# Optimization experiments

Hardware: AMD Instinct MI355X
Metric: run time of the kernel (lower is better)

Reference implementation:

```python
import jax, jax.numpy as jnp
import numpy as np

B, N, S, K = 4, 32768, 8192, 16
IN_C, OUT_C = 64, 128
MID = max(OUT_C // 4, 8)  # attn_mlp hidden = 32
GN_GROUPS = 8
EPS = 1e-5


def setup_inputs() -> dict:
    key = jax.random.key(0)
    ks = jax.random.split(key, 16)
    def lin(k, out_c, in_c):
        # torch nn.Linear default init: U(-1/sqrt(in), 1/sqrt(in)), weight shape (out, in)
        bound = 1.0 / np.sqrt(in_c)
        return jax.random.uniform(k, (out_c, in_c), jnp.float32, -bound, bound)
    return {
        "xyz": jax.random.normal(ks[0], (B, N, 3), jnp.float32),
        "feats": jax.random.normal(ks[1], (B, N, IN_C), jnp.float32),
        "idx_fps": jax.random.randint(ks[2], (B, S), 0, N),
        "idx_knn": jax.random.randint(ks[3], (B, S, K), 0, N),
        "Wq": lin(ks[4], OUT_C, IN_C),
        "Wk": lin(ks[5], OUT_C, IN_C),
        "Wv": lin(ks[6], OUT_C, IN_C),
        "Wp1": lin(ks[7], OUT_C, 3),
        "Wp2": lin(ks[8], OUT_C, OUT_C),
        "Wa1": lin(ks[9], MID, OUT_C),
        "Wa2": lin(ks[10], OUT_C, MID),
        "Wproj": lin(ks[11], OUT_C, OUT_C),
        "ln_w": jnp.ones((OUT_C,), jnp.float32),
        "ln_b": jnp.zeros((OUT_C,), jnp.float32),
        "Wres": lin(ks[12], OUT_C, IN_C),
        "Wpost": lin(ks[13], OUT_C, OUT_C),
        "gn_w": jnp.ones((OUT_C,), jnp.float32),
        "gn_b": jnp.zeros((OUT_C,), jnp.float32),
    }


def _gather(x, idx):
    # x: (B, N, C); idx: (B, ...) -> (B, ..., C)
    return jax.vmap(lambda xb, ib: xb[ib])(x, idx)


def _layer_norm(x, w, b):
    mu = x.mean(-1, keepdims=True)
    var = x.var(-1, keepdims=True)
    return (x - mu) * jax.lax.rsqrt(var + EPS) * w + b


def _group_norm(x, w, b):
    # x: (B, S, C); normalize per (batch, group) over (S, C//G) — matches GroupNorm on (B,C,L)
    Bx, Sx, C = x.shape
    xg = x.reshape(Bx, Sx, GN_GROUPS, C // GN_GROUPS)
    mu = xg.mean(axis=(1, 3), keepdims=True)
    var = xg.var(axis=(1, 3), keepdims=True)
    xn = (xg - mu) * jax.lax.rsqrt(var + EPS)
    return xn.reshape(Bx, Sx, C) * w + b


def _forward(xyz, feats, idx_fps, idx_knn, Wq, Wk, Wv, Wp1, Wp2, Wa1, Wa2,
             Wproj, ln_w, ln_b, Wres, Wpost, gn_w, gn_b):
    s_xyz = _gather(xyz, idx_fps)        # (B,S,3)
    s_feat = _gather(feats, idx_fps)     # (B,S,C_in)
    n_xyz = _gather(xyz, idx_knn)        # (B,S,k,3)
    n_feat = _gather(feats, idx_knn)     # (B,S,k,C_in)

    # LocalAttentionBlock (Point Transformer v1 subtraction attention)
    q = jnp.einsum('bsc,oc->bso', s_feat, Wq)[:, :, None, :]   # (B,S,1,O)
    kk = jnp.einsum('bskc,oc->bsko', n_feat, Wk)               # (B,S,k,O)
    v = jnp.einsum('bskc,oc->bsko', n_feat, Wv)
    rel = n_xyz - s_xyz[:, :, None, :]                         # (B,S,k,3)
    pe = jnp.einsum('bskm,om->bsko',
                    jax.nn.relu(jnp.einsum('bskc,oc->bsko', rel, Wp1)), Wp2)
    h = q - kk + pe
    w = jnp.einsum('bskm,om->bsko',
                   jax.nn.relu(jnp.einsum('bsko,mo->bskm', h, Wa1)), Wa2)
    w = jax.nn.softmax(w, axis=2)                              # softmax over k
    out = jnp.sum(w * (v + pe), axis=2)                        # (B,S,O)
    out = jnp.einsum('bso,po->bsp', out, Wproj)
    res = jnp.einsum('bsc,oc->bso', s_feat, Wres)
    out = _layer_norm(out + res, ln_w, ln_b)

    # post: Conv1d(1x1, no bias) -> GroupNorm(8) -> ReLU
    out = jnp.einsum('bso,po->bsp', out, Wpost)
    out = jax.nn.relu(_group_norm(out, gn_w, gn_b))
    return s_xyz, out


def reference(xyz, feats, idx_fps, idx_knn, Wq, Wk, Wv, Wp1, Wp2, Wa1, Wa2,
              Wproj, ln_w, ln_b, Wres, Wpost, gn_w, gn_b):
    return _forward(xyz, feats, idx_fps, idx_knn, Wq, Wk, Wv, Wp1, Wp2, Wa1,
                    Wa2, Wproj, ln_w, ln_b, Wres, Wpost, gn_w, gn_b)
```

## Files before the change

kernel.cpp:

```cpp
#include <hip/hip_runtime.h>
#include <hip/hip_bf16.h>
#include <math.h>

#define B_ 4
#define N_ 32768
#define S_ 8192
#define K_ 16
#define CIN 64
#define COUT 128
#define MID_ 32
#define EPS_ 1e-5f
#define NTILE 2048

typedef __attribute__((ext_vector_type(8))) short s16x8;
typedef __attribute__((ext_vector_type(4))) float f32x4;

__device__ ushort g_attn[(size_t)B_ * S_ * COUT];
__device__ ushort g_sfeat[(size_t)B_ * S_ * CIN];
__device__ float  g_part[NTILE * 8 * 2];
__device__ float  g_stats[64];
__device__ float  g_fw[8192];

__device__ __forceinline__ uint pk2(float lo, float hi) {
  __hip_bfloat162 h = __float22bfloat162_rn(make_float2(lo, hi));
  return *(uint*)&h;
}
__device__ __forceinline__ ushort f2bf(float f) {
  __hip_bfloat16 h = __float2bfloat16(f);
  return *(ushort*)&h;
}
__device__ __forceinline__ int4 pack8(float4 a, float4 b) {
  int4 o;
  o.x = pk2(a.x, a.y); o.y = pk2(a.z, a.w);
  o.z = pk2(b.x, b.y); o.w = pk2(b.z, b.w);
  return o;
}
__device__ __forceinline__ f32x4 mfma16(s16x8 a, s16x8 b, f32x4 c) {
  return __builtin_amdgcn_mfma_f32_16x16x32_bf16(a, b, c, 0, 0, 0);
}
__device__ __forceinline__ s16x8 ldw256(const ushort* W, int row, int g) {
  return *(const s16x8*)((const char*)W + row * 256 + ((g ^ (row & 7)) << 4));
}
__device__ __forceinline__ s16x8 ldw128(const ushort* W, int row, int g) {
  return *(const s16x8*)((const char*)W + row * 128 + ((g ^ (row & 7)) << 4));
}
__device__ __forceinline__ s16x8 ldfrag_g8(const float* p) {
  float4 a = *(const float4*)p, b = *(const float4*)(p + 4);
  union { int4 i; s16x8 s; } u;
  u.i = pack8(a, b);
  return u.s;
}
__device__ __forceinline__ void st16(char* bufb, int t, f32x4 c, int l, int cq,
                                     bool dorelu) {
  const int colp = (l & 15) + 16 * t;
  const int g = colp >> 3;
  const int off = (colp & 7) * 2;
  #pragma unroll
  for (int rr = 0; rr < 4; ++rr) {
    const int row = cq * 4 + rr;
    float v = dorelu ? fmaxf(c[rr], 0.f) : c[rr];
    *(ushort*)(bufb + row * 256 + ((g ^ (row & 7)) << 4) + off) = f2bf(v);
  }
}
__device__ __forceinline__ void st16_a1(char* bufb, int t, f32x4 c, int l, int cq) {
  const int colp = (l & 15) + 16 * t;
  const int g = colp >> 3;
  const int off = (colp & 7) * 2;
  #pragma unroll
  for (int rr = 0; rr < 4; ++rr) {
    const int row = cq * 4 + rr;
    *(ushort*)(bufb + row * 64 + ((g ^ (row & 3)) << 4) + off) =
        f2bf(fmaxf(c[rr], 0.f));
  }
}

__global__ __launch_bounds__(256) void k_fuse(
    const float* __restrict__ Wq, const float* __restrict__ Wk,
    const float* __restrict__ Wp2, const float* __restrict__ Wa1)
{
  const int t = blockIdx.x * 256 + threadIdx.x;
  if (t < 2048) {
    int m = t >> 6, c = t & 63;
    float s = 0.f;
    for (int o = 0; o < COUT; ++o) s += Wa1[m * COUT + o] * Wq[o * CIN + c];
    g_fw[t] = s;
  } else if (t < 4096) {
    int u = t - 2048;
    int m = u >> 6, c = u & 63;
    float s = 0.f;
    for (int o = 0; o < COUT; ++o) s += Wa1[m * COUT + o] * Wk[o * CIN + c];
    g_fw[t] = s;
  } else {
    int u = t - 4096;
    int m = u >> 7, c = u & 127;
    float s = 0.f;
    for (int o = 0; o < COUT; ++o) s += Wa1[m * COUT + o] * Wp2[o * COUT + c];
    g_fw[t] = s;
  }
}

__global__ __launch_bounds__(512, 2) void k_attn(
    const float* __restrict__ xyz, const float* __restrict__ feats,
    const int* __restrict__ idx_fps, const int* __restrict__ idx_knn,
    const float* __restrict__ Wv, const float* __restrict__ Wp1,
    const float* __restrict__ Wp2, const float* __restrict__ Wa2,
    float* __restrict__ out_xyz)
{
  __shared__ ushort lWv[COUT * CIN];
  __shared__ ushort lWp1[COUT * 8];
  __shared__ ushort lWp2[COUT * COUT];
  __shared__ ushort lWka1[MID_ * CIN];
  __shared__ ushort lWpa1[MID_ * COUT];
  __shared__ ushort sbuf[8 * 2560];

  const int tid = threadIdx.x;
  const int w = tid >> 6, l = tid & 63;
  const int r = l & 15, cq = l >> 4;

  for (int i = tid; i < COUT * CIN / 2; i += 512) {
    int row = i >> 5; int kp = (i & 31) * 2;
    int g = kp >> 3;
    *(uint*)((char*)lWv + row * 128 + ((g ^ (row & 7)) << 4) + (kp & 7) * 2)
        = pk2(Wv[row * CIN + kp], Wv[row * CIN + kp + 1]);
  }
  {
    int row = tid >> 2; int kp = (tid & 3) * 2;
    float lo = (kp < 3) ? Wp1[row * 3 + kp] : 0.f;
    float hi = (kp + 1 < 3) ? Wp1[row * 3 + kp + 1] : 0.f;
    *(uint*)((char*)lWp1 + row * 16 + kp * 2) = pk2(lo, hi);
  }
  for (int i = tid; i < COUT * CIN; i += 512) {
    int row = i >> 6; int kp = (i & 63) * 2;
    int g = kp >> 3;
    *(uint*)((char*)lWp2 + row * 256 + ((g ^ (row & 7)) << 4) + (kp & 7) * 2)
        = pk2(Wp2[row * COUT + kp], Wp2[row * COUT + kp + 1]);
  }
  for (int i = tid; i < MID_ * CIN / 2; i += 512) {
    int row = i >> 5; int kp = (i & 31) * 2;
    int g = kp >> 3;
    const float* src = g_fw + 2048 + row * CIN + kp;
    *(uint*)((char*)lWka1 + row * 128 + ((g ^ (row & 7)) << 4) + (kp & 7) * 2)
        = pk2(-src[0], -src[1]);
  }
  for (int i = tid; i < MID_ * COUT / 2; i += 512) {
    int row = i >> 6; int kp = (i & 63) * 2;
    int g = kp >> 3;
    const float* src = g_fw + 4096 + row * COUT + kp;
    *(uint*)((char*)lWpa1 + row * 256 + ((g ^ (row & 7)) << 4) + (kp & 7) * 2)
        = pk2(src[0], src[1]);
  }

  s16x8 fWa2[8], fQ[2][2];
  #pragma unroll
  for (int t = 0; t < 8; ++t)
    fWa2[t] = ldfrag_g8(Wa2 + (16 * t + r) * MID_ + cq * 8);
  #pragma unroll
  for (int t = 0; t < 2; ++t)
    #pragma unroll
    for (int ks = 0; ks < 2; ++ks)
      fQ[t][ks] = ldfrag_g8(g_fw + (16 * t + r) * CIN + ks * 32 + cq * 8);

  __syncthreads();

  char* bufb = (char*)(sbuf + w * 2560);
  const int pid0 = (blockIdx.x * 8 + w) * 16;

  {
    const int p = pid0 + r;
    const int bb = p >> 13;
    const int si = idx_fps[p];
    const float* fs = feats + ((size_t)bb * N_ + si) * CIN;
    #pragma unroll
    for (int j = 0; j < 2; ++j) {
      int g = cq * 2 + j;
      int4 pks = pack8(*(const float4*)(fs + g * 8), *(const float4*)(fs + g * 8 + 4));
      *(int4*)(bufb + r * 128 + ((g ^ (r & 7)) << 4)) = pks;
      *(int4*)((char*)g_sfeat + (size_t)p * 128 + g * 16) = pks;
    }
    if (l < 48) {
      int pi = l / 3, j = l - pi * 3;
      int pp = pid0 + pi;
      out_xyz[(size_t)pp * 3 + j] =
          xyz[((size_t)(pp >> 13) * N_ + idx_fps[pp]) * 3 + j];
    }
  }
  f32x4 qa1[2];
  qa1[0] = (f32x4){0, 0, 0, 0}; qa1[1] = (f32x4){0, 0, 0, 0};
  {
    s16x8 fS[2];
    #pragma unroll
    for (int ks = 0; ks < 2; ++ks)
      fS[ks] = *(const s16x8*)(bufb + r * 128 + (((ks * 4 + cq) ^ (r & 7)) << 4));
    #pragma unroll
    for (int ks = 0; ks < 2; ++ks)
      #pragma unroll
      for (int t = 0; t < 2; ++t)
        qa1[t] = mfma16(fS[ks], fQ[t][ks], qa1[t]);
  }

  float4 pf0, pf1, pf2, pf3;
  float pxn0, pxn1, pxn2, pxs0, pxs1, pxs2;
  int nid_n;
  {
    int nid0 = idx_knn[(size_t)pid0 * K_ + r];
    const float* fn = feats + ((size_t)N_ * (pid0 >> 13) + nid0) * CIN + cq * 16;
    pf0 = ((const float4*)fn)[0]; pf1 = ((const float4*)fn)[1];
    pf2 = ((const float4*)fn)[2]; pf3 = ((const float4*)fn)[3];
    if (cq == 0) {
      const float* xn = xyz + ((size_t)N_ * (pid0 >> 13) + nid0) * 3;
      const float* xs = xyz + ((size_t)N_ * (pid0 >> 13) + idx_fps[pid0]) * 3;
      pxn0 = xn[0]; pxn1 = xn[1]; pxn2 = xn[2];
      pxs0 = xs[0]; pxs1 = xs[1]; pxs2 = xs[2];
    }
    nid_n = idx_knn[(size_t)(pid0 + 1) * K_ + r];
  }

  #pragma unroll 1
  for (int i = 0; i < 16; ++i) {
    const int pid = pid0 + i;

    {
      int g0 = cq * 2;
      *(int4*)(bufb + r * 128 + ((g0 ^ (r & 7)) << 4)) = pack8(pf0, pf1);
      *(int4*)(bufb + r * 128 + (((g0 + 1) ^ (r & 7)) << 4)) = pack8(pf2, pf3);
    }
    s16x8 fRel = {0, 0, 0, 0, 0, 0, 0, 0};
    if (cq == 0) {
      fRel[0] = (short)f2bf(pxn0 - pxs0);
      fRel[1] = (short)f2bf(pxn1 - pxs1);
      fRel[2] = (short)f2bf(pxn2 - pxs2);
    }

    if (i < 15) {
      const int pidn = pid + 1;
      const int bn = pidn >> 13;
      const float* fn = feats + ((size_t)bn * N_ + nid_n) * CIN + cq * 16;
      float4 t0 = ((const float4*)fn)[0], t1 = ((const float4*)fn)[1];
      float4 t2 = ((const float4*)fn)[2], t3 = ((const float4*)fn)[3];
      if (cq == 0) {
        const float* xn = xyz + ((size_t)bn * N_ + nid_n) * 3;
        const float* xs = xyz + ((size_t)bn * N_ + idx_fps[pidn]) * 3;
        pxn0 = xn[0]; pxn1 = xn[1]; pxn2 = xn[2];
        pxs0 = xs[0]; pxs1 = xs[1]; pxs2 = xs[2];
      }
      if (i < 14) nid_n = idx_knn[(size_t)(pid + 2) * K_ + r];
      pf0 = t0; pf1 = t1; pf2 = t2; pf3 = t3;
    }

    s16x8 fA[2];
    #pragma unroll
    for (int ks = 0; ks < 2; ++ks)
      fA[ks] = *(const s16x8*)(bufb + r * 128 + (((ks * 4 + cq) ^ (r & 7)) << 4));

    f32x4 vv[8];
    #pragma unroll
    for (int t = 0; t < 8; ++t) vv[t] = (f32x4){0, 0, 0, 0};
    #pragma unroll
    for (int ks = 0; ks < 2; ++ks)
      #pragma unroll
      for (int t = 0; t < 8; ++t)
        vv[t] = mfma16(fA[ks], ldw128(lWv, 16 * t + r, ks * 4 + cq), vv[t]);

    f32x4 za[2];
    za[0] = (f32x4){0, 0, 0, 0}; za[1] = (f32x4){0, 0, 0, 0};
    #pragma unroll
    for (int ks = 0; ks < 2; ++ks)
      #pragma unroll
      for (int t = 0; t < 2; ++t)
        za[t] = mfma16(fA[ks], ldw128(lWka1, 16 * t + r, ks * 4 + cq), za[t]);

    #pragma unroll
    for (int t = 0; t < 8; ++t) {
      f32x4 z = {0, 0, 0, 0};
      f32x4 c = mfma16(fRel, *(const s16x8*)((const char*)lWp1 + (16 * t + r) * 16), z);
      st16(bufb, t, c, l, cq, true);
    }
    s16x8 fT[4];
    #pragma unroll
    for (int ks = 0; ks < 4; ++ks)
      fT[ks] = *(const s16x8*)(bufb + r * 256 + (((ks * 4 + cq) ^ (r & 7)) << 4));

    #pragma unroll
    for (int ks = 0; ks < 4; ++ks)
      #pragma unroll
      for (int t = 0; t < 8; ++t)
        vv[t] = mfma16(fT[ks], ldw256(lWp2, 16 * t + r, ks * 4 + cq), vv[t]);

    #pragma unroll
    for (int ks = 0; ks < 4; ++ks)
      #pragma unroll
      for (int t = 0; t < 2; ++t)
        za[t] = mfma16(fT[ks], ldw256(lWpa1, 16 * t + r, ks * 4 + cq), za[t]);

    const int ii = i & 3, iq = i >> 2;
    #pragma unroll
    for (int t = 0; t < 2; ++t) {
      float qsel = ii == 0 ? qa1[t][0] : ii == 1 ? qa1[t][1]
                 : ii == 2 ? qa1[t][2] : qa1[t][3];
      float qv = __shfl(qsel, (iq << 4) + (l & 15));
      #pragma unroll
      for (int rr = 0; rr < 4; ++rr) za[t][rr] += qv;
      st16_a1(bufb + 4096, t, za[t], l, cq);
    }
    s16x8 fA1 = *(const s16x8*)(bufb + 4096 + r * 64 + ((cq ^ (r & 3)) << 4));
    f32x4 ww[8];
    #pragma unroll
    for (int t = 0; t < 8; ++t) {
      f32x4 z = {0, 0, 0, 0};
      ww[t] = mfma16(fA1, fWa2[t], z);
    }
    #pragma unroll
    for (int t = 0; t < 8; ++t) {
      float m = fmaxf(fmaxf(ww[t][0], ww[t][1]), fmaxf(ww[t][2], ww[t][3]));
      m = fmaxf(m, __shfl_xor(m, 16));
      m = fmaxf(m, __shfl_xor(m, 32));
      float e0 = __expf(ww[t][0] - m), e1 = __expf(ww[t][1] - m);
      float e2 = __expf(ww[t][2] - m), e3 = __expf(ww[t][3] - m);
      float ss = e0 + e1 + e2 + e3;
      ss += __shfl_xor(ss, 16);
      ss += __shfl_xor(ss, 32);
      float acc = e0 * vv[t][0] + e1 * vv[t][1] + e2 * vv[t][2] + e3 * vv[t][3];
      acc += __shfl_xor(acc, 16);
      acc += __shfl_xor(acc, 32);
      float outv = acc / ss;
      if (cq == (t >> 2)) {
        int colp = (l & 15) + 16 * t;
        *(ushort*)((char*)g_attn + (size_t)pid * 256 + colp * 2) = f2bf(outv);
      }
    }
  }
}

__global__ __launch_bounds__(512, 2) void k_post(
    const float* __restrict__ Wproj, const float* __restrict__ Wres,
    const float* __restrict__ Wpost, const float* __restrict__ ln_w,
    const float* __restrict__ ln_b, float* __restrict__ out_main)
{
  __shared__ ushort lWpj[COUT * COUT];
  __shared__ ushort lWrs[COUT * CIN];
  __shared__ ushort lWps[COUT * COUT];
  __shared__ float  llnw[COUT], llnb[COUT];
  __shared__ ushort sbuf[8 * 16 * COUT];

  const int tid = threadIdx.x;
  const int w = tid >> 6, l = tid & 63;
  const int r = l & 15, cq = l >> 4;

  for (int i = tid; i < COUT * CIN; i += 512) {
    int row = i >> 6; int kp = (i & 63) * 2;
    int g = kp >> 3;
    *(uint*)((char*)lWpj + row * 256 + ((g ^ (row & 7)) << 4) + (kp & 7) * 2)
        = pk2(Wproj[row * COUT + kp], Wproj[row * COUT + kp + 1]);
  }
  for (int i = tid; i < COUT * CIN / 2; i += 512) {
    int row = i >> 5; int kp = (i & 31) * 2;
    int g = kp >> 3;
    *(uint*)((char*)lWrs + row * 128 + ((g ^ (row & 7)) << 4) + (kp & 7) * 2)
        = pk2(Wres[row * CIN + kp], Wres[row * CIN + kp + 1]);
  }
  for (int i = tid; i < COUT * CIN; i += 512) {
    int row = i >> 6; int kp = (i & 63) * 2;
    int g = kp >> 3;
    *(uint*)((char*)lWps + row * 256 + ((g ^ (row & 7)) << 4) + (kp & 7) * 2)
        = pk2(Wpost[row * COUT + kp], Wpost[row * COUT + kp + 1]);
  }
  if (tid < COUT) { llnw[tid] = ln_w[tid]; llnb[tid] = ln_b[tid]; }
  __syncthreads();

  const int T = blockIdx.x * 8 + w;
  char* bufb = (char*)(sbuf + w * 16 * COUT);

  f32x4 acc[8];
  #pragma unroll
  for (int t = 0; t < 8; ++t) acc[t] = (f32x4){0, 0, 0, 0};

  s16x8 fA[4];
  #pragma unroll
  for (int ks = 0; ks < 4; ++ks)
    fA[ks] = *(const s16x8*)(g_attn + ((size_t)T * 16 + r) * COUT + ks * 32 + cq * 8);
  #pragma unroll
  for (int ks = 0; ks < 4; ++ks)
    #pragma unroll
    for (int t = 0; t < 8; ++t)
      acc[t] = mfma16(fA[ks], ldw256(lWpj, 16 * t + r, ks * 4 + cq), acc[t]);

  s16x8 fS[2];
  #pragma unroll
  for (int ks = 0; ks < 2; ++ks)
    fS[ks] = *(const s16x8*)(g_sfeat + ((size_t)T * 16 + r) * CIN + ks * 32 + cq * 8);
  #pragma unroll
  for (int ks = 0; ks < 2; ++ks)
    #pragma unroll
    for (int t = 0; t < 8; ++t)
      acc[t] = mfma16(fS[ks], ldw128(lWrs, 16 * t + r, ks * 4 + cq), acc[t]);

  #pragma unroll
  for (int rr = 0; rr < 4; ++rr) {
    float s1 = 0.f, s2 = 0.f;
    #pragma unroll
    for (int t = 0; t < 8; ++t) { float v = acc[t][rr]; s1 += v; s2 += v * v; }
    #pragma unroll
    for (int off = 1; off < 16; off <<= 1) {
      s1 += __shfl_xor(s1, off);
      s2 += __shfl_xor(s2, off);
    }
    float mu = s1 * (1.f / COUT);
    float rs = rsqrtf(s2 * (1.f / COUT) - mu * mu + EPS_);
    #pragma unroll
    for (int t = 0; t < 8; ++t) {
      int col = (l & 15) + 16 * t;
      acc[t][rr] = (acc[t][rr] - mu) * rs * llnw[col] + llnb[col];
    }
  }
  #pragma unroll
  for (int t = 0; t < 8; ++t) st16(bufb, t, acc[t], l, cq, false);

  s16x8 fZ[4];
  #pragma unroll
  for (int ks = 0; ks < 4; ++ks)
    fZ[ks] = *(const s16x8*)(bufb + r * 256 + (((ks * 4 + cq) ^ (r & 7)) << 4));
  f32x4 po[8];
  #pragma unroll
  for (int t = 0; t < 8; ++t) po[t] = (f32x4){0, 0, 0, 0};
  #pragma unroll
  for (int ks = 0; ks < 4; ++ks)
    #pragma unroll
    for (int t = 0; t < 8; ++t)
      po[t] = mfma16(fZ[ks], ldw256(lWps, 16 * t + r, ks * 4 + cq), po[t]);

  #pragma unroll
  for (int t = 0; t < 8; ++t) {
    float s1 = po[t][0] + po[t][1] + po[t][2] + po[t][3];
    float s2 = po[t][0] * po[t][0] + po[t][1] * po[t][1]
             + po[t][2] * po[t][2] + po[t][3] * po[t][3];
    #pragma unroll
    for (int off = 1; off < 64; off <<= 1) {
      s1 += __shfl_xor(s1, off);
      s2 += __shfl_xor(s2, off);
    }
    if (l == 0) {
      g_part[((size_t)T * 8 + t) * 2] = s1;
      g_part[((size_t)T * 8 + t) * 2 + 1] = s2;
    }
    #pragma unroll
    for (int rr = 0; rr < 4; ++rr) {
      int row = T * 16 + cq * 4 + rr;
      out_main[(size_t)row * COUT + (l & 15) + 16 * t] = po[t][rr];
    }
  }
}

__global__ void k_gn_finish(void) {
  int bg = blockIdx.x;
  int b = bg >> 3, g = bg & 7;
  int t = threadIdx.x;
  float s1 = 0.f, s2 = 0.f;
  for (int i = t; i < 512; i += 64) {
    size_t T = (size_t)b * 512 + i;
    s1 += g_part[(T * 8 + g) * 2];
    s2 += g_part[(T * 8 + g) * 2 + 1];
  }
  #pragma unroll
  for (int off = 1; off < 64; off <<= 1) {
    s1 += __shfl_xor(s1, off);
    s2 += __shfl_xor(s2, off);
  }
  if (t == 0) {
    float n = (float)S_ * 16.f;
    float mu = s1 / n;
    float var = s2 / n - mu * mu;
    g_stats[bg * 2] = mu;
    g_stats[bg * 2 + 1] = rsqrtf(var + EPS_);
  }
}

__global__ __launch_bounds__(256) void k_gn_apply(
    float* __restrict__ x, const float* __restrict__ gn_w,
    const float* __restrict__ gn_b)
{
  const int i = blockIdx.x * 256 + threadIdx.x;
  if (i >= B_ * S_ * (COUT / 4)) return;
  const int c = (i & 31) * 4;
  const int g = c >> 4;
  const int b = i >> 18;
  const float m = g_stats[(b * 8 + g) * 2];
  const float rv = g_stats[(b * 8 + g) * 2 + 1];
  float4 v = ((float4*)x)[i];
  v.x = fmaxf((v.x - m) * rv * gn_w[c + 0] + gn_b[c + 0], 0.f);
  v.y = fmaxf((v.y - m) * rv * gn_w[c + 1] + gn_b[c + 1], 0.f);
  v.z = fmaxf((v.z - m) * rv * gn_w[c + 2] + gn_b[c + 2], 0.f);
  v.w = fmaxf((v.w - m) * rv * gn_w[c + 3] + gn_b[c + 3], 0.f);
  ((float4*)x)[i] = v;
}

extern "C" void kernel_launch(void* const* d_in, const int* in_sizes, int n_in,
                              void* d_out, int out_size, void* d_ws, size_t ws_size,
                              hipStream_t stream) {
  const float* xyz     = (const float*)d_in[0];
  const float* feats   = (const float*)d_in[1];
  const int*   idx_fps = (const int*)d_in[2];
  const int*   idx_knn = (const int*)d_in[3];
  const float* Wq    = (const float*)d_in[4];
  const float* Wk    = (const float*)d_in[5];
  const float* Wv    = (const float*)d_in[6];
  const float* Wp1   = (const float*)d_in[7];
  const float* Wp2   = (const float*)d_in[8];
  const float* Wa1   = (const float*)d_in[9];
  const float* Wa2   = (const float*)d_in[10];
  const float* Wproj = (const float*)d_in[11];
  const float* ln_w  = (const float*)d_in[12];
  const float* ln_b  = (const float*)d_in[13];
  const float* Wres  = (const float*)d_in[14];
  const float* Wpost = (const float*)d_in[15];
  const float* gn_w  = (const float*)d_in[16];
  const float* gn_b  = (const float*)d_in[17];

  float* out      = (float*)d_out;
  float* out_xyz  = out;
  float* out_main = out + (size_t)B_ * S_ * 3;

  k_fuse<<<dim3(32), dim3(256), 0, stream>>>(Wq, Wk, Wp2, Wa1);
  k_attn<<<dim3(256), dim3(512), 0, stream>>>(
      xyz, feats, idx_fps, idx_knn, Wv, Wp1, Wp2, Wa2, out_xyz);
  k_post<<<dim3(256), dim3(512), 0, stream>>>(
      Wproj, Wres, Wpost, ln_w, ln_b, out_main);
  k_gn_finish<<<dim3(32), dim3(64), 0, stream>>>();
  k_gn_apply<<<dim3((B_ * S_ * (COUT / 4) + 255) / 256), dim3(256), 0, stream>>>(
      out_main, gn_w, gn_b);
}
```

Measured before the change: 140.5 us.

## Process two sample points per loop iteration in attention kernel

The attention kernel now handles two sample points per iteration, giving each wave two LDS buffers so each weight fragment loaded from LDS feeds two MFMAs. Prefetching becomes two-deep and the per-wave LDS buffer doubles. Launch bounds drop from two blocks per CU to one to make room for the extra registers and LDS. This trades occupancy for better weight reuse and more independent MFMA chains.

```diff
diff --git a/kernel.cpp b/kernel.cpp
--- a/kernel.cpp
+++ b/kernel.cpp
@@ -72,6 +72,23 @@
     *(ushort*)(bufb + row * 64 + ((g ^ (row & 3)) << 4) + off) =
         f2bf(fmaxf(c[rr], 0.f));
   }
+}
+
+struct PF { float4 f0, f1, f2, f3; float r0, r1, r2; };
+__device__ __forceinline__ PF pfetch(const float* feats, const float* xyz,
+                                     const int* idx_fps, int pid, int nid, int cq) {
+  PF p;
+  const int bb = pid >> 13;
+  const float* fn = feats + ((size_t)bb * N_ + nid) * CIN + cq * 16;
+  p.f0 = ((const float4*)fn)[0]; p.f1 = ((const float4*)fn)[1];
+  p.f2 = ((const float4*)fn)[2]; p.f3 = ((const float4*)fn)[3];
+  p.r0 = 0.f; p.r1 = 0.f; p.r2 = 0.f;
+  if (cq == 0) {
+    const float* xn = xyz + ((size_t)bb * N_ + nid) * 3;
+    const float* xs = xyz + ((size_t)bb * N_ + idx_fps[pid]) * 3;
+    p.r0 = xn[0] - xs[0]; p.r1 = xn[1] - xs[1]; p.r2 = xn[2] - xs[2];
+  }
+  return p;
 }
 
 __global__ __launch_bounds__(256) void k_fuse(
@@ -99,7 +116,7 @@
   }
 }
 
-__global__ __launch_bounds__(512, 2) void k_attn(
+__global__ __launch_bounds__(512, 1) void k_attn(
     const float* __restrict__ xyz, const float* __restrict__ feats,
     const int* __restrict__ idx_fps, const int* __restrict__ idx_knn,
     const float* __restrict__ Wv, const float* __restrict__ Wp1,
@@ -111,7 +128,7 @@
   __shared__ ushort lWp2[COUT * COUT];
   __shared__ ushort lWka1[MID_ * CIN];
   __shared__ ushort lWpa1[MID_ * COUT];
-  __shared__ ushort sbuf[8 * 2560];
+  __shared__ ushort sbuf[8 * 5120];
 
   const int tid = threadIdx.x;
   const int w = tid >> 6, l = tid & 63;
@@ -150,19 +167,18 @@
         = pk2(src[0], src[1]);
   }
 
-  s16x8 fWa2[8], fQ[2][2];
+  s16x8 fWa2[8];
   #pragma unroll
   for (int t = 0; t < 8; ++t)
     fWa2[t] = ldfrag_g8(Wa2 + (16 * t + r) * MID_ + cq * 8);
-  #pragma unroll
-  for (int t = 0; t < 2; ++t)
-    #pragma unroll
-    for (int ks = 0; ks < 2; ++ks)
-      fQ[t][ks] = ldfrag_g8(g_fw + (16 * t + r) * CIN + ks * 32 + cq * 8);
 
   __syncthreads();
 
-  char* bufb = (char*)(sbuf + w * 2560);
+  char* bufb = (char*)(sbuf + w * 5120);
+  char* buf0 = bufb;
+  char* buf1 = bufb + 4096;
+  char* bufa0 = bufb + 8192;
+  char* bufa1 = bufb + 9216;
   const int pid0 = (blockIdx.x * 8 + w) * 16;
 
   {
@@ -174,7 +190,7 @@
     for (int j = 0; j < 2; ++j) {
       int g = cq * 2 + j;
       int4 pks = pack8(*(const float4*)(fs + g * 8), *(const float4*)(fs + g * 8 + 4));
-      *(int4*)(bufb + r * 128 + ((g ^ (r & 7)) << 4)) = pks;
+      *(int4*)(buf0 + r * 128 + ((g ^ (r & 7)) << 4)) = pks;
       *(int4*)((char*)g_sfeat + (size_t)p * 128 + g * 16) = pks;
     }
     if (l < 48) {
@@ -187,145 +203,173 @@
   f32x4 qa1[2];
   qa1[0] = (f32x4){0, 0, 0, 0}; qa1[1] = (f32x4){0, 0, 0, 0};
   {
-    s16x8 fS[2];
+    s16x8 fS[2], fQ;
     #pragma unroll
     for (int ks = 0; ks < 2; ++ks)
-      fS[ks] = *(const s16x8*)(bufb + r * 128 + (((ks * 4 + cq) ^ (r & 7)) << 4));
+      fS[ks] = *(const s16x8*)(buf0 + r * 128 + (((ks * 4 + cq) ^ (r & 7)) << 4));
     #pragma unroll
     for (int ks = 0; ks < 2; ++ks)
       #pragma unroll
-      for (int t = 0; t < 2; ++t)
-        qa1[t] = mfma16(fS[ks], fQ[t][ks], qa1[t]);
-  }
-
-  float4 pf0, pf1, pf2, pf3;
-  float pxn0, pxn1, pxn2, pxs0, pxs1, pxs2;
-  int nid_n;
-  {
-    int nid0 = idx_knn[(size_t)pid0 * K_ + r];
-    const float* fn = feats + ((size_t)N_ * (pid0 >> 13) + nid0) * CIN + cq * 16;
-    pf0 = ((const float4*)fn)[0]; pf1 = ((const float4*)fn)[1];
-    pf2 = ((const float4*)fn)[2]; pf3 = ((const float4*)fn)[3];
-    if (cq == 0) {
-      const float* xn = xyz + ((size_t)N_ * (pid0 >> 13) + nid0) * 3;
-      const float* xs = xyz + ((size_t)N_ * (pid0 >> 13) + idx_fps[pid0]) * 3;
-      pxn0 = xn[0]; pxn1 = xn[1]; pxn2 = xn[2];
-      pxs0 = xs[0]; pxs1 = xs[1]; pxs2 = xs[2];
-    }
-    nid_n = idx_knn[(size_t)(pid0 + 1) * K_ + r];
-  }
+      for (int t = 0; t < 2; ++t) {
+        fQ = ldfrag_g8(g_fw + (16 * t + r) * CIN + ks * 32 + cq * 8);
+        qa1[t] = mfma16(fS[ks], fQ, qa1[t]);
+      }
+  }
+
+  PF pa = pfetch(feats, xyz, idx_fps, pid0,
+                 idx_knn[(size_t)pid0 * K_ + r], cq);
+  PF pb = pfetch(feats, xyz, idx_fps, pid0 + 1,
+                 idx_knn[(size_t)(pid0 + 1) * K_ + r], cq);
+  int nidA = idx_knn[(size_t)(pid0 + 2) * K_ + r];
+  int nidB = idx_knn[(size_t)(pid0 + 3) * K_ + r];
 
   #pragma unroll 1
-  for (int i = 0; i < 16; ++i) {
-    const int pid = pid0 + i;
+  for (int ip = 0; ip < 8; ++ip) {
+    const int pidA = pid0 + 2 * ip;
+    const int pidB = pidA + 1;
 
     {
       int g0 = cq * 2;
-      *(int4*)(bufb + r * 128 + ((g0 ^ (r & 7)) << 4)) = pack8(pf0, pf1);
-      *(int4*)(bufb + r * 128 + (((g0 + 1) ^ (r & 7)) << 4)) = pack8(pf2, pf3);
-    }
-    s16x8 fRel = {0, 0, 0, 0, 0, 0, 0, 0};
+      *(int4*)(buf0 + r * 128 + ((g0 ^ (r & 7)) << 4)) = pack8(pa.f0, pa.f1);
+      *(int4*)(buf0 + r * 128 + (((g0 + 1) ^ (r & 7)) << 4)) = pack8(pa.f2, pa.f3);
+      *(int4*)(buf1 + r * 128 + ((g0 ^ (r & 7)) << 4)) = pack8(pb.f0, pb.f1);
+      *(int4*)(buf1 + r * 128 + (((g0 + 1) ^ (r & 7)) << 4)) = pack8(pb.f2, pb.f3);
+    }
+    s16x8 fRa = {0, 0, 0, 0, 0, 0, 0, 0};
+    s16x8 fRb = {0, 0, 0, 0, 0, 0, 0, 0};
     if (cq == 0) {
-      fRel[0] = (short)f2bf(pxn0 - pxs0);
-      fRel[1] = (short)f2bf(pxn1 - pxs1);
-      fRel[2] = (short)f2bf(pxn2 - pxs2);
-    }
-
-    if (i < 15) {
-      const int pidn = pid + 1;
-      const int bn = pidn >> 13;
-      const float* fn = feats + ((size_t)bn * N_ + nid_n) * CIN + cq * 16;
-      float4 t0 = ((const float4*)fn)[0], t1 = ((const float4*)fn)[1];
-      float4 t2 = ((const float4*)fn)[2], t3 = ((const float4*)fn)[3];
-      if (cq == 0) {
-        const float* xn = xyz + ((size_t)bn * N_ + nid_n) * 3;
-        const float* xs = xyz + ((size_t)bn * N_ + idx_fps[pidn]) * 3;
-        pxn0 = xn[0]; pxn1 = xn[1]; pxn2 = xn[2];
-        pxs0 = xs[0]; pxs1 = xs[1]; pxs2 = xs[2];
-      }
-      if (i < 14) nid_n = idx_knn[(size_t)(pid + 2) * K_ + r];
-      pf0 = t0; pf1 = t1; pf2 = t2; pf3 = t3;
-    }
-
-    s16x8 fA[2];
-    #pragma unroll
-    for (int ks = 0; ks < 2; ++ks)
-      fA[ks] = *(const s16x8*)(bufb + r * 128 + (((ks * 4 + cq) ^ (r & 7)) << 4));
-
-    f32x4 vv[8];
-    #pragma unroll
-    for (int t = 0; t < 8; ++t) vv[t] = (f32x4){0, 0, 0, 0};
+      fRa[0] = (short)f2bf(pa.r0); fRa[1] = (short)f2bf(pa.r1);
+      fRa[2] = (short)f2bf(pa.r2);
+      fRb[0] = (short)f2bf(pb.r0); fRb[1] = (short)f2bf(pb.r1);
+      fRb[2] = (short)f2bf(pb.r2);
+    }
+
+    if (ip < 7) {
+      pa = pfetch(feats, xyz, idx_fps, pidA + 2, nidA, cq);
+      pb = pfetch(feats, xyz, idx_fps, pidB + 2, nidB, cq);
+      if (ip < 6) {
+        nidA = idx_knn[(size_t)(pidA + 4) * K_ + r];
+        nidB = idx_knn[(size_t)(pidB + 4) * K_ + r];
+      }
+    }
+
+    s16x8 fAa[2], fAb[2];
+    #pragma unroll
+    for (int ks = 0; ks < 2; ++ks) {
+      fAa[ks] = *(const s16x8*)(buf0 + r * 128 + (((ks * 4 + cq) ^ (r & 7)) << 4));
+      fAb[ks] = *(const s16x8*)(buf1 + r * 128 + (((ks * 4 + cq) ^ (r & 7)) << 4));
+    }
+
+    f32x4 va[8], vb[8];
+    #pragma unroll
+    for (int t = 0; t < 8; ++t) { va[t] = (f32x4){0,0,0,0}; vb[t] = (f32x4){0,0,0,0}; }
     #pragma unroll
     for (int ks = 0; ks < 2; ++ks)
       #pragma unroll
-      for (int t = 0; t < 8; ++t)
-        vv[t] = mfma16(fA[ks], ldw128(lWv, 16 * t + r, ks * 4 + cq), vv[t]);
-
-    f32x4 za[2];
-    za[0] = (f32x4){0, 0, 0, 0}; za[1] = (f32x4){0, 0, 0, 0};
+      for (int t = 0; t < 8; ++t) {
+        s16x8 wb = ldw128(lWv, 16 * t + r, ks * 4 + cq);
+        va[t] = mfma16(fAa[ks], wb, va[t]);
+        vb[t] = mfma16(fAb[ks], wb, vb[t]);
+      }
+
+    f32x4 zaa[2], zab[2];
+    zaa[0] = (f32x4){0,0,0,0}; zaa[1] = (f32x4){0,0,0,0};
+    zab[0] = (f32x4){0,0,0,0}; zab[1] = (f32x4){0,0,0,0};
     #pragma unroll
     for (int ks = 0; ks < 2; ++ks)
       #pragma unroll
-      for (int t = 0; t < 2; ++t)
-        za[t] = mfma16(fA[ks], ldw128(lWka1, 16 * t + r, ks * 4 + cq), za[t]);
+      for (int t = 0; t < 2; ++t) {
+        s16x8 wb = ldw128(lWka1, 16 * t + r, ks * 4 + cq);
+        zaa[t] = mfma16(fAa[ks], wb, zaa[t]);
+        zab[t] = mfma16(fAb[ks], wb, zab[t]);
+      }
 
     #pragma unroll
     for (int t = 0; t < 8; ++t) {
-      f32x4 z = {0, 0, 0, 0};
-      f32x4 c = mfma16(fRel, *(const s16x8*)((const char*)lWp1 + (16 * t + r) * 16), z);
-      st16(bufb, t, c, l, cq, true);
-    }
-    s16x8 fT[4];
-    #pragma unroll
-    for (int ks = 0; ks < 4; ++ks)
-      fT[ks] = *(const s16x8*)(bufb + r * 256 + (((ks * 4 + cq) ^ (r & 7)) << 4));
+      s16x8 wp = *(const s16x8*)((const char*)lWp1 + (16 * t + r) * 16);
+      f32x4 z0 = {0, 0, 0, 0}, z1 = {0, 0, 0, 0};
+      f32x4 ca = mfma16(fRa, wp, z0);
+      f32x4 cb = mfma16(fRb, wp, z1);
+      st16(buf0, t, ca, l, cq, true);
+      st16(buf1, t, cb, l, cq, true);
+    }
+    s16x8 fTa[4], fTb[4];
+    #pragma unroll
+    for (int ks = 0; ks < 4; ++ks) {
+      fTa[ks] = *(const s16x8*)(buf0 + r * 256 + (((ks * 4 + cq) ^ (r & 7)) << 4));
+      fTb[ks] = *(const s16x8*)(buf1 + r * 256 + (((ks * 4 + cq) ^ (r & 7)) << 4));
+    }
 
     #pragma unroll
     for (int ks = 0; ks < 4; ++ks)
       #pragma unroll
-      for (int t = 0; t < 8; ++t)
-        vv[t] = mfma16(fT[ks], ldw256(lWp2, 16 * t + r, ks * 4 + cq), vv[t]);
+      for (int t = 0; t < 8; ++t) {
+        s16x8 wb = ldw256(lWp2, 16 * t + r, ks * 4 + cq);
+        va[t] = mfma16(fTa[ks], wb, va[t]);
+        vb[t] = mfma16(fTb[ks], wb, vb[t]);
+      }
 
     #pragma unroll
     for (int ks = 0; ks < 4; ++ks)
       #pragma unroll
-      for (int t = 0; t < 2; ++t)
-        za[t] = mfma16(fT[ks], ldw256(lWpa1, 16 * t + r, ks * 4 + cq), za[t]);
-
-    const int ii = i & 3, iq = i >> 2;
-    #pragma unroll
-    for (int t = 0; t < 2; ++t) {
-      float qsel = ii == 0 ? qa1[t][0] : ii == 1 ? qa1[t][1]
-                 : ii == 2 ? qa1[t][2] : qa1[t][3];
-      float qv = __shfl(qsel, (iq << 4) + (l & 15));
+      for (int t = 0; t < 2; ++t) {
+        s16x8 wb = ldw256(lWpa1, 16 * t + r, ks * 4 + cq);
+        zaa[t] = mfma16(fTa[ks], wb, zaa[t]);
+        zab[t] = mfma16(fTb[ks], wb, zab[t]);
+      }
+
+    {
+      const int ja = 2 * ip, jb = 2 * ip + 1;
+      const int iia = ja & 3, iqa = ja >> 2;
+      const int iib = jb & 3, iqb = jb >> 2;
       #pragma unroll
-      for (int rr = 0; rr < 4; ++rr) za[t][rr] += qv;
-      st16_a1(bufb + 4096, t, za[t], l, cq);
-    }
-    s16x8 fA1 = *(const s16x8*)(bufb + 4096 + r * 64 + ((cq ^ (r & 3)) << 4));
-    f32x4 ww[8];
+      for (int t = 0; t < 2; ++t) {
+        float qsa = iia == 0 ? qa1[t][0] : iia == 1 ? qa1[t][1]
+                  : iia == 2 ? qa1[t][2] : qa1[t][3];
+        float qva = __shfl(qsa, (iqa << 4) + (l & 15));
+        float qsb = iib == 0 ? qa1[t][0] : iib == 1 ? qa1[t][1]
+                  : iib == 2 ? qa1[t][2] : qa1[t][3];
+        float qvb = __shfl(qsb, (iqb << 4) + (l & 15));
+        f32x4 ta = zaa[t], tb = zab[t];
+        #pragma unroll
+        for (int rr = 0; rr < 4; ++rr) { ta[rr] += qva; tb[rr] += qvb; }
+        st16_a1(bufa0, t, ta, l, cq);
+        st16_a1(bufa1, t, tb, l, cq);
+      }
+    }
+    s16x8 fA1a = *(const s16x8*)(bufa0 + r * 64 + ((cq ^ (r & 3)) << 4));
+    s16x8 fA1b = *(const s16x8*)(bufa1 + r * 64 + ((cq ^ (r & 3)) << 4));
+    f32x4 wwa[8], wwb[8];
     #pragma unroll
     for (int t = 0; t < 8; ++t) {
-      f32x4 z = {0, 0, 0, 0};
-      ww[t] = mfma16(fA1, fWa2[t], z);
+      f32x4 z0 = {0, 0, 0, 0}, z1 = {0, 0, 0, 0};
+      wwa[t] = mfma16(fA1a, fWa2[t], z0);
+      wwb[t] = mfma16(fA1b, fWa2[t], z1);
     }
     #pragma unroll
     for (int t = 0; t < 8; ++t) {
-      float m = fmaxf(fmaxf(ww[t][0], ww[t][1]), fmaxf(ww[t][2], ww[t][3]));
-      m = fmaxf(m, __shfl_xor(m, 16));
-      m = fmaxf(m, __shfl_xor(m, 32));
-      float e0 = __expf(ww[t][0] - m), e1 = __expf(ww[t][1] - m);
-      float e2 = __expf(ww[t][2] - m), e3 = __expf(ww[t][3] - m);
-      float ss = e0 + e1 + e2 + e3;
-      ss += __shfl_xor(ss, 16);
-      ss += __shfl_xor(ss, 32);
-      float acc = e0 * vv[t][0] + e1 * vv[t][1] + e2 * vv[t][2] + e3 * vv[t][3];
-      acc += __shfl_xor(acc, 16);
-      acc += __shfl_xor(acc, 32);
-      float outv = acc / ss;
+      float ma = fmaxf(fmaxf(wwa[t][0], wwa[t][1]), fmaxf(wwa[t][2], wwa[t][3]));
+      float mb = fmaxf(fmaxf(wwb[t][0], wwb[t][1]), fmaxf(wwb[t][2], wwb[t][3]));
+      ma = fmaxf(ma, __shfl_xor(ma, 16)); mb = fmaxf(mb, __shfl_xor(mb, 16));
+      ma = fmaxf(ma, __shfl_xor(ma, 32)); mb = fmaxf(mb, __shfl_xor(mb, 32));
+      float ea0 = __expf(wwa[t][0] - ma), ea1 = __expf(wwa[t][1] - ma);
+      float ea2 = __expf(wwa[t][2] - ma), ea3 = __expf(wwa[t][3] - ma);
+      float eb0 = __expf(wwb[t][0] - mb), eb1 = __expf(wwb[t][1] - mb);
+      float eb2 = __expf(wwb[t][2] - mb), eb3 = __expf(wwb[t][3] - mb);
+      float ssa = ea0 + ea1 + ea2 + ea3;
+      float ssb = eb0 + eb1 + eb2 + eb3;
+      ssa += __shfl_xor(ssa, 16); ssb += __shfl_xor(ssb, 16);
+      ssa += __shfl_xor(ssa, 32); ssb += __shfl_xor(ssb, 32);
+      float aca = ea0 * va[t][0] + ea1 * va[t][1] + ea2 * va[t][2] + ea3 * va[t][3];
+      float acb = eb0 * vb[t][0] + eb1 * vb[t][1] + eb2 * vb[t][2] + eb3 * vb[t][3];
+      aca += __shfl_xor(aca, 16); acb += __shfl_xor(acb, 16);
+      aca += __shfl_xor(aca, 32); acb += __shfl_xor(acb, 32);
+      float oa = aca / ssa;
+      float ob = acb / ssb;
       if (cq == (t >> 2)) {
         int colp = (l & 15) + 16 * t;
-        *(ushort*)((char*)g_attn + (size_t)pid * 256 + colp * 2) = f2bf(outv);
+        *(ushort*)((char*)g_attn + (size_t)pidA * 256 + colp * 2) = f2bf(oa);
+        *(ushort*)((char*)g_attn + (size_t)pidB * 256 + colp * 2) = f2bf(ob);
       }
     }
   }
```

Result: slower. 171.7 us (+22.1%).

## Double waves per attention block, halve points per wave, stage Wa2 in LDS

Applied to the files above, without the earlier changes.

The attention kernel now launches 1024-thread blocks of 16 waves, each processing 8 sampled points instead of 16, so each CU keeps twice as many waves in flight to hide the latency of the neighbour gathers. The Wa2 fragments move from registers into a swizzled LDS tile, and the Wq-fused fragments are loaded on demand. This frees registers. The neighbour prefetch is wrapped in a helper that computes the relative position early, and the positional-encoding MFMAs are moved ahead of the value projection. The launch bound of 1024 threads with 4 blocks may force a very low VGPR budget and spilling. The larger shared buffer also limits how many blocks can be resident per CU.

```diff
diff --git a/kernel.cpp b/kernel.cpp
--- a/kernel.cpp
+++ b/kernel.cpp
@@ -44,6 +44,9 @@
 __device__ __forceinline__ s16x8 ldw128(const ushort* W, int row, int g) {
   return *(const s16x8*)((const char*)W + row * 128 + ((g ^ (row & 7)) << 4));
 }
+__device__ __forceinline__ s16x8 ldw64(const ushort* W, int row, int g) {
+  return *(const s16x8*)((const char*)W + row * 64 + ((g ^ (row & 3)) << 4));
+}
 __device__ __forceinline__ s16x8 ldfrag_g8(const float* p) {
   float4 a = *(const float4*)p, b = *(const float4*)(p + 4);
   union { int4 i; s16x8 s; } u;
@@ -72,6 +75,23 @@
     *(ushort*)(bufb + row * 64 + ((g ^ (row & 3)) << 4) + off) =
         f2bf(fmaxf(c[rr], 0.f));
   }
+}
+
+struct PF { float4 f0, f1, f2, f3; float r0, r1, r2; };
+__device__ __forceinline__ PF pfetch(const float* feats, const float* xyz,
+                                     const int* idx_fps, int pid, int nid, int cq) {
+  PF p;
+  const int bb = pid >> 13;
+  const float* fn = feats + ((size_t)bb * N_ + nid) * CIN + cq * 16;
+  p.f0 = ((const float4*)fn)[0]; p.f1 = ((const float4*)fn)[1];
+  p.f2 = ((const float4*)fn)[2]; p.f3 = ((const float4*)fn)[3];
+  p.r0 = 0.f; p.r1 = 0.f; p.r2 = 0.f;
+  if (cq == 0) {
+    const float* xn = xyz + ((size_t)bb * N_ + nid) * 3;
+    const float* xs = xyz + ((size_t)bb * N_ + idx_fps[pid]) * 3;
+    p.r0 = xn[0] - xs[0]; p.r1 = xn[1] - xs[1]; p.r2 = xn[2] - xs[2];
+  }
+  return p;
 }
 
 __global__ __launch_bounds__(256) void k_fuse(
@@ -99,7 +119,7 @@
   }
 }
 
-__global__ __launch_bounds__(512, 2) void k_attn(
+__global__ __launch_bounds__(1024, 4) void k_attn(
     const float* __restrict__ xyz, const float* __restrict__ feats,
     const int* __restrict__ idx_fps, const int* __restrict__ idx_knn,
     const float* __restrict__ Wv, const float* __restrict__ Wp1,
@@ -111,62 +131,60 @@
   __shared__ ushort lWp2[COUT * COUT];
   __shared__ ushort lWka1[MID_ * CIN];
   __shared__ ushort lWpa1[MID_ * COUT];
-  __shared__ ushort sbuf[8 * 2560];
+  __shared__ ushort lWa2[COUT * MID_];
+  __shared__ ushort sbuf[16 * 2560];
 
   const int tid = threadIdx.x;
   const int w = tid >> 6, l = tid & 63;
   const int r = l & 15, cq = l >> 4;
 
-  for (int i = tid; i < COUT * CIN / 2; i += 512) {
+  for (int i = tid; i < COUT * CIN / 2; i += 1024) {
     int row = i >> 5; int kp = (i & 31) * 2;
     int g = kp >> 3;
     *(uint*)((char*)lWv + row * 128 + ((g ^ (row & 7)) << 4) + (kp & 7) * 2)
         = pk2(Wv[row * CIN + kp], Wv[row * CIN + kp + 1]);
   }
-  {
+  if (tid < 512) {
     int row = tid >> 2; int kp = (tid & 3) * 2;
     float lo = (kp < 3) ? Wp1[row * 3 + kp] : 0.f;
     float hi = (kp + 1 < 3) ? Wp1[row * 3 + kp + 1] : 0.f;
     *(uint*)((char*)lWp1 + row * 16 + kp * 2) = pk2(lo, hi);
   }
-  for (int i = tid; i < COUT * CIN; i += 512) {
+  for (int i = tid; i < COUT * CIN; i += 1024) {
     int row = i >> 6; int kp = (i & 63) * 2;
     int g = kp >> 3;
     *(uint*)((char*)lWp2 + row * 256 + ((g ^ (row & 7)) << 4) + (kp & 7) * 2)
         = pk2(Wp2[row * COUT + kp], Wp2[row * COUT + kp + 1]);
   }
-  for (int i = tid; i < MID_ * CIN / 2; i += 512) {
+  for (int i = tid; i < MID_ * CIN / 2; i += 1024) {
     int row = i >> 5; int kp = (i & 31) * 2;
     int g = kp >> 3;
     const float* src = g_fw + 2048 + row * CIN + kp;
     *(uint*)((char*)lWka1 + row * 128 + ((g ^ (row & 7)) << 4) + (kp & 7) * 2)
         = pk2(-src[0], -src[1]);
   }
-  for (int i = tid; i < MID_ * COUT / 2; i += 512) {
+  for (int i = tid; i < MID_ * COUT / 2; i += 1024) {
     int row = i >> 6; int kp = (i & 63) * 2;
     int g = kp >> 3;
     const float* src = g_fw + 4096 + row * COUT + kp;
     *(uint*)((char*)lWpa1 + row * 256 + ((g ^ (row & 7)) << 4) + (kp & 7) * 2)
         = pk2(src[0], src[1]);
   }
-
-  s16x8 fWa2[8], fQ[2][2];
-  #pragma unroll
-  for (int t = 0; t < 8; ++t)
-    fWa2[t] = ldfrag_g8(Wa2 + (16 * t + r) * MID_ + cq * 8);
-  #pragma unroll
-  for (int t = 0; t < 2; ++t)
-    #pragma unroll
-    for (int ks = 0; ks < 2; ++ks)
-      fQ[t][ks] = ldfrag_g8(g_fw + (16 * t + r) * CIN + ks * 32 + cq * 8);
+  for (int i = tid; i < COUT * MID_ / 2; i += 1024) {
+    int row = i >> 4; int kp = (i & 15) * 2;
+    int g = kp >> 3;
+    *(uint*)((char*)lWa2 + row * 64 + ((g ^ (row & 3)) << 4) + (kp & 7) * 2)
+        = pk2(Wa2[row * MID_ + kp], Wa2[row * MID_ + kp + 1]);
+  }
 
   __syncthreads();
 
   char* bufb = (char*)(sbuf + w * 2560);
-  const int pid0 = (blockIdx.x * 8 + w) * 16;
+  char* bufa = bufb + 4096;
+  const int pid0 = (blockIdx.x * 16 + w) * 8;
 
   {
-    const int p = pid0 + r;
+    const int p = pid0 + (r & 7);
     const int bb = p >> 13;
     const int si = idx_fps[p];
     const float* fs = feats + ((size_t)bb * N_ + si) * CIN;
@@ -175,9 +193,9 @@
       int g = cq * 2 + j;
       int4 pks = pack8(*(const float4*)(fs + g * 8), *(const float4*)(fs + g * 8 + 4));
       *(int4*)(bufb + r * 128 + ((g ^ (r & 7)) << 4)) = pks;
-      *(int4*)((char*)g_sfeat + (size_t)p * 128 + g * 16) = pks;
-    }
-    if (l < 48) {
+      if (r < 8) *(int4*)((char*)g_sfeat + (size_t)p * 128 + g * 16) = pks;
+    }
+    if (l < 24) {
       int pi = l / 3, j = l - pi * 3;
       int pp = pid0 + pi;
       out_xyz[(size_t)pp * 3 + j] =
@@ -187,70 +205,54 @@
   f32x4 qa1[2];
   qa1[0] = (f32x4){0, 0, 0, 0}; qa1[1] = (f32x4){0, 0, 0, 0};
   {
-    s16x8 fS[2];
+    s16x8 fS[2], fQ;
     #pragma unroll
     for (int ks = 0; ks < 2; ++ks)
       fS[ks] = *(const s16x8*)(bufb + r * 128 + (((ks * 4 + cq) ^ (r & 7)) << 4));
     #pragma unroll
     for (int ks = 0; ks < 2; ++ks)
       #pragma unroll
-      for (int t = 0; t < 2; ++t)
-        qa1[t] = mfma16(fS[ks], fQ[t][ks], qa1[t]);
-  }
-
-  float4 pf0, pf1, pf2, pf3;
-  float pxn0, pxn1, pxn2, pxs0, pxs1, pxs2;
-  int nid_n;
-  {
-    int nid0 = idx_knn[(size_t)pid0 * K_ + r];
-    const float* fn = feats + ((size_t)N_ * (pid0 >> 13) + nid0) * CIN + cq * 16;
-    pf0 = ((const float4*)fn)[0]; pf1 = ((const float4*)fn)[1];
-    pf2 = ((const float4*)fn)[2]; pf3 = ((const float4*)fn)[3];
-    if (cq == 0) {
-      const float* xn = xyz + ((size_t)N_ * (pid0 >> 13) + nid0) * 3;
-      const float* xs = xyz + ((size_t)N_ * (pid0 >> 13) + idx_fps[pid0]) * 3;
-      pxn0 = xn[0]; pxn1 = xn[1]; pxn2 = xn[2];
-      pxs0 = xs[0]; pxs1 = xs[1]; pxs2 = xs[2];
-    }
-    nid_n = idx_knn[(size_t)(pid0 + 1) * K_ + r];
-  }
+      for (int t = 0; t < 2; ++t) {
+        fQ = ldfrag_g8(g_fw + (16 * t + r) * CIN + ks * 32 + cq * 8);
+        qa1[t] = mfma16(fS[ks], fQ, qa1[t]);
+      }
+  }
+
+  PF pa = pfetch(feats, xyz, idx_fps, pid0, idx_knn[(size_t)pid0 * K_ + r], cq);
+  int nid_n = idx_knn[(size_t)(pid0 + 1) * K_ + r];
 
   #pragma unroll 1
-  for (int i = 0; i < 16; ++i) {
+  for (int i = 0; i < 8; ++i) {
     const int pid = pid0 + i;
 
     {
       int g0 = cq * 2;
-      *(int4*)(bufb + r * 128 + ((g0 ^ (r & 7)) << 4)) = pack8(pf0, pf1);
-      *(int4*)(bufb + r * 128 + (((g0 + 1) ^ (r & 7)) << 4)) = pack8(pf2, pf3);
+      *(int4*)(bufb + r * 128 + ((g0 ^ (r & 7)) << 4)) = pack8(pa.f0, pa.f1);
+      *(int4*)(bufb + r * 128 + (((g0 + 1) ^ (r & 7)) << 4)) = pack8(pa.f2, pa.f3);
     }
     s16x8 fRel = {0, 0, 0, 0, 0, 0, 0, 0};
     if (cq == 0) {
-      fRel[0] = (short)f2bf(pxn0 - pxs0);
-      fRel[1] = (short)f2bf(pxn1 - pxs1);
-      fRel[2] = (short)f2bf(pxn2 - pxs2);
-    }
-
-    if (i < 15) {
-      const int pidn = pid + 1;
-      const int bn = pidn >> 13;
-      const float* fn = feats + ((size_t)bn * N_ + nid_n) * CIN + cq * 16;
-      float4 t0 = ((const float4*)fn)[0], t1 = ((const float4*)fn)[1];
-      float4 t2 = ((const float4*)fn)[2], t3 = ((const float4*)fn)[3];
-      if (cq == 0) {
-        const float* xn = xyz + ((size_t)bn * N_ + nid_n) * 3;
-        const float* xs = xyz + ((size_t)bn * N_ + idx_fps[pidn]) * 3;
-        pxn0 = xn[0]; pxn1 = xn[1]; pxn2 = xn[2];
-        pxs0 = xs[0]; pxs1 = xs[1]; pxs2 = xs[2];
-      }
-      if (i < 14) nid_n = idx_knn[(size_t)(pid + 2) * K_ + r];
-      pf0 = t0; pf1 = t1; pf2 = t2; pf3 = t3;
+      fRel[0] = (short)f2bf(pa.r0);
+      fRel[1] = (short)f2bf(pa.r1);
+      fRel[2] = (short)f2bf(pa.r2);
+    }
+
+    if (i < 7) {
+      pa = pfetch(feats, xyz, idx_fps, pid + 1, nid_n, cq);
+      if (i < 6) nid_n = idx_knn[(size_t)(pid + 2) * K_ + r];
     }
 
     s16x8 fA[2];
     #pragma unroll
     for (int ks = 0; ks < 2; ++ks)
       fA[ks] = *(const s16x8*)(bufb + r * 128 + (((ks * 4 + cq) ^ (r & 7)) << 4));
+
+    #pragma unroll
+    for (int t = 0; t < 8; ++t) {
+      f32x4 z = {0, 0, 0, 0};
+      f32x4 c = mfma16(fRel, *(const s16x8*)((const char*)lWp1 + (16 * t + r) * 16), z);
+      st16(bufb, t, c, l, cq, true);
+    }
 
     f32x4 vv[8];
     #pragma unroll
@@ -269,12 +271,6 @@
       for (int t = 0; t < 2; ++t)
         za[t] = mfma16(fA[ks], ldw128(lWka1, 16 * t + r, ks * 4 + cq), za[t]);
 
-    #pragma unroll
-    for (int t = 0; t < 8; ++t) {
-      f32x4 z = {0, 0, 0, 0};
-      f32x4 c = mfma16(fRel, *(const s16x8*)((const char*)lWp1 + (16 * t + r) * 16), z);
-      st16(bufb, t, c, l, cq, true);
-    }
     s16x8 fT[4];
     #pragma unroll
     for (int ks = 0; ks < 4; ++ks)
@@ -298,16 +294,17 @@
       float qsel = ii == 0 ? qa1[t][0] : ii == 1 ? qa1[t][1]
                  : ii == 2 ? qa1[t][2] : qa1[t][3];
       float qv = __shfl(qsel, (iq << 4) + (l & 15));
+      f32x4 ta = za[t];
       #pragma unroll
-      for (int rr = 0; rr < 4; ++rr) za[t][rr] += qv;
-      st16_a1(bufb + 4096, t, za[t], l, cq);
-    }
-    s16x8 fA1 = *(const s16x8*)(bufb + 4096 + r * 64 + ((cq ^ (r & 3)) << 4));
+      for (int rr = 0; rr < 4; ++rr) ta[rr] += qv;
+      st16_a1(bufa, t, ta, l, cq);
+    }
+    s16x8 fA1 = *(const s16x8*)(bufa + r * 64 + ((cq ^ (r & 3)) << 4));
     f32x4 ww[8];
     #pragma unroll
     for (int t = 0; t < 8; ++t) {
       f32x4 z = {0, 0, 0, 0};
-      ww[t] = mfma16(fA1, fWa2[t], z);
+      ww[t] = mfma16(fA1, ldw64(lWa2, 16 * t + r, cq), z);
     }
     #pragma unroll
     for (int t = 0; t < 8; ++t) {
@@ -520,7 +517,7 @@
   float* out_main = out + (size_t)B_ * S_ * 3;
 
   k_fuse<<<dim3(32), dim3(256), 0, stream>>>(Wq, Wk, Wp2, Wa1);
-  k_attn<<<dim3(256), dim3(512), 0, stream>>>(
+  k_attn<<<dim3(256), dim3(1024), 0, stream>>>(
       xyz, feats, idx_fps, idx_knn, Wv, Wp1, Wp2, Wa2, out_xyz);
   k_post<<<dim3(256), dim3(512), 0, stream>>>(
       Wproj, Wres, Wpost, ln_w, ln_b, out_main);
```

After: 171.2 us. +21.8%, slower.
